# Optimization experiments

Measured on AMD Instinct MI355X. Metric: run time of the kernel, lower is better.

The kernel has to match this reference:

```python
import jax, jax.numpy as jnp
import numpy as np

N_NODES = 50000
N_EDGES = 800000
D_IN = 64
D_OUT = 64


def setup_inputs() -> dict:
    key = jax.random.key(0)
    ks = jax.random.split(key, 5)
    feat = jax.random.normal(ks[0], (N_NODES, D_IN), dtype=jnp.float32)
    src = jax.random.randint(ks[1], (N_EDGES,), 0, N_NODES, dtype=jnp.int64)
    dst = jax.random.randint(ks[2], (N_EDGES,), 0, N_NODES, dtype=jnp.int64)
    # Xavier-uniform-ish scale for weights
    lim = float(np.sqrt(6.0 / (D_IN + D_OUT)) * np.sqrt(2.0))
    W_neigh = jax.random.uniform(ks[3], (D_OUT, D_IN), dtype=jnp.float32, minval=-lim, maxval=lim)
    W_self = jax.random.uniform(ks[4], (D_OUT, D_IN), dtype=jnp.float32, minval=-lim, maxval=lim)
    b_self = jnp.zeros((D_OUT,), dtype=jnp.float32)
    return {"feat": feat, "src": src, "dst": dst,
            "W_neigh": W_neigh, "W_self": W_self, "b_self": b_self}


def reference(feat, src, dst, W_neigh, W_self, b_self):
    # srcdata = fc_neigh(feat_src)  -> [N, D_OUT]
    srcdata = feat @ W_neigh.T
    # A_div.T @ srcdata == mean of transformed source feats over in-edges per dst.
    # deg[j] = A.sum(0)[j]; column scaling by 1/deg then transpose-SpMM.
    agg = jax.ops.segment_sum(srcdata[src], dst, num_segments=N_NODES)  # [N, D_OUT]
    deg = jax.ops.segment_sum(jnp.ones_like(dst, dtype=srcdata.dtype), dst,
                              num_segments=N_NODES)  # [N]
    # Zero-degree columns stay zero in the sparse product (no stored nonzeros).
    dstdata = jnp.where(deg[:, None] > 0, agg / jnp.maximum(deg, 1.0)[:, None], 0.0)
    # rst = fc_self(feat_dst) + dstdata ; feat_dst = feat[:N_dst] = feat (square A)
    return feat @ W_self.T + b_self + dstdata
```

## Files before the change

### kernel.cpp

```cpp
#include <hip/hip_runtime.h>

#define N_NODES 50000
#define N_EDGES 800000
#define D 64
#define RB 128
#define NBUCK 391
#define CAP 3072
#define PAD 16
#define NFEATBLK 3125

typedef __attribute__((ext_vector_type(8))) __bf16 bf16x8;
typedef __attribute__((ext_vector_type(4))) float f32x4;
typedef __attribute__((ext_vector_type(2))) float f32x2;

__device__ inline unsigned f2bf(float f) {
    unsigned b = __builtin_bit_cast(unsigned, f);
    b += 0x7fffu + ((b >> 16) & 1u);
    return b >> 16;
}

__global__ __launch_bounds__(256) void pre_kernel(const float* __restrict__ feat,
                                                  const float* __restrict__ Wn,
                                                  const float* __restrict__ Ws,
                                                  unsigned short* __restrict__ fb,
                                                  unsigned* __restrict__ fq,
                                                  unsigned short* __restrict__ wnb,
                                                  unsigned short* __restrict__ wsb) {
    int b = blockIdx.x;
    int t = threadIdx.x;
    if (b < NFEATBLK) {
        int i = b * 256 + t;
        float4 v = ((const float4*)feat)[i];
        uint2 o;
        o.x = f2bf(v.x) | (f2bf(v.y) << 16);
        o.y = f2bf(v.z) | (f2bf(v.w) << 16);
        ((uint2*)fb)[i] = o;
        int q = __builtin_amdgcn_cvt_pk_fp8_f32(v.x, v.y, 0, false);
        q = __builtin_amdgcn_cvt_pk_fp8_f32(v.z, v.w, q, true);
        fq[i] = (unsigned)q;
    } else {
        for (int i = t; i < D * D; i += 256) {
            wnb[i] = (unsigned short)f2bf(Wn[i]);
            wsb[i] = (unsigned short)f2bf(Ws[i]);
        }
    }
}

__global__ __launch_bounds__(1024) void passB_kernel(const int* __restrict__ src, const int* __restrict__ dst,
                                                     int* __restrict__ bcursor, unsigned int* __restrict__ ebuf) {
    __shared__ int cnt[NBUCK];
    __shared__ int base[NBUCK];
    int t = threadIdx.x;
    for (int i = t; i < NBUCK; i += 1024) cnt[i] = 0;
    __syncthreads();
    int eb = blockIdx.x * 8192;
    int s_[8], b_[8], dl_[8];
#pragma unroll
    for (int k = 0; k < 8; ++k) {
        int e = eb + k * 1024 + t;
        if (e < N_EDGES) {
            int dv = dst[e];
            s_[k] = src[e];
            b_[k] = dv >> 7;
            dl_[k] = dv & (RB - 1);
            atomicAdd(&cnt[b_[k]], 1);
        } else b_[k] = -1;
    }
    __syncthreads();
    for (int i = t; i < NBUCK; i += 1024) {
        int c = cnt[i];
        base[i] = c ? atomicAdd(&bcursor[i * PAD], c) : 0;
    }
    __syncthreads();
#pragma unroll
    for (int k = 0; k < 8; ++k) {
        if (b_[k] >= 0) {
            int pos = atomicAdd(&base[b_[k]], 1);
            if (pos < CAP)
                ebuf[(size_t)b_[k] * CAP + pos] = (unsigned)s_[k] | ((unsigned)dl_[k] << 16);
        }
    }
}

__global__ __launch_bounds__(256) void sort_kernel(const int* __restrict__ bcursor,
                                                   const unsigned int* __restrict__ ebuf,
                                                   unsigned short* __restrict__ es2,
                                                   int* __restrict__ offs, int* __restrict__ degA) {
    __shared__ int cnt[RB];
    __shared__ int sc[RB];
    __shared__ int cur[RB];
    int t = threadIdx.x;
    int bk = blockIdx.x;
    if (t < RB) cnt[t] = 0;
    __syncthreads();
    int s0 = bk * CAP;
    int n = bcursor[bk * PAD];
    if (n > CAP) n = CAP;
    for (int i = t; i < n; i += 256) atomicAdd(&cnt[ebuf[s0 + i] >> 16], 1);
    __syncthreads();
    int c = (t < RB) ? cnt[t] : 0;
    if (t < RB) sc[t] = c;
    __syncthreads();
    for (int d = 1; d < RB; d <<= 1) {
        int v = (t < RB && t >= d) ? sc[t - d] : 0;
        __syncthreads();
        if (t < RB) sc[t] += v;
        __syncthreads();
    }
    if (t < RB) {
        int ex = sc[t] - c;
        cur[t] = ex;
        int node = bk * RB + t;
        if (node < N_NODES) { offs[node] = s0 + ex; degA[node] = c; }
    }
    __syncthreads();
    for (int i = t; i < n; i += 256) {
        unsigned r = ebuf[s0 + i];
        int p = atomicAdd(&cur[r >> 16], 1);
        es2[s0 + p] = (unsigned short)(r & 0xFFFFu);
    }
}

#define ALD 68
__global__ __launch_bounds__(256) void gather_mfma_kernel(
        const unsigned short* __restrict__ fb, const unsigned char* __restrict__ fq,
        const int* __restrict__ offs, const int* __restrict__ degA,
        const unsigned short* __restrict__ es2,
        const unsigned short* __restrict__ wsb, const unsigned short* __restrict__ wnb,
        const float* __restrict__ bias, float* __restrict__ out) {
    __shared__ float agg[16 * ALD];
    int t = threadIdx.x;
    int w = t >> 6, lane = t & 63;
    int es = lane >> 3, p = lane & 7;
    int r0 = blockIdx.x * 16;
#pragma unroll
    for (int q = 0; q < 4; ++q) {
        int nl = w * 4 + q;
        int r = r0 + nl;
        int dg = degA[r];
        int start = offs[r];
        float acc[8] = {0.f, 0.f, 0.f, 0.f, 0.f, 0.f, 0.f, 0.f};
        int i = 0;
        for (; i + 16 <= dg; i += 16) {
            unsigned id0 = es2[start + i + es];
            unsigned id1 = es2[start + i + 8 + es];
            uint2 q0 = *(const uint2*)(fq + (size_t)id0 * D + p * 8);
            uint2 q1 = *(const uint2*)(fq + (size_t)id1 * D + p * 8);
            f32x2 a;
            a = __builtin_amdgcn_cvt_pk_f32_fp8((int)q0.x, false); acc[0] += a.x; acc[1] += a.y;
            a = __builtin_amdgcn_cvt_pk_f32_fp8((int)q0.x, true);  acc[2] += a.x; acc[3] += a.y;
            a = __builtin_amdgcn_cvt_pk_f32_fp8((int)q0.y, false); acc[4] += a.x; acc[5] += a.y;
            a = __builtin_amdgcn_cvt_pk_f32_fp8((int)q0.y, true);  acc[6] += a.x; acc[7] += a.y;
            a = __builtin_amdgcn_cvt_pk_f32_fp8((int)q1.x, false); acc[0] += a.x; acc[1] += a.y;
            a = __builtin_amdgcn_cvt_pk_f32_fp8((int)q1.x, true);  acc[2] += a.x; acc[3] += a.y;
            a = __builtin_amdgcn_cvt_pk_f32_fp8((int)q1.y, false); acc[4] += a.x; acc[5] += a.y;
            a = __builtin_amdgcn_cvt_pk_f32_fp8((int)q1.y, true);  acc[6] += a.x; acc[7] += a.y;
        }
        for (; i + 8 <= dg; i += 8) {
            unsigned id = es2[start + i + es];
            uint2 qv = *(const uint2*)(fq + (size_t)id * D + p * 8);
            f32x2 a;
            a = __builtin_amdgcn_cvt_pk_f32_fp8((int)qv.x, false); acc[0] += a.x; acc[1] += a.y;
            a = __builtin_amdgcn_cvt_pk_f32_fp8((int)qv.x, true);  acc[2] += a.x; acc[3] += a.y;
            a = __builtin_amdgcn_cvt_pk_f32_fp8((int)qv.y, false); acc[4] += a.x; acc[5] += a.y;
            a = __builtin_amdgcn_cvt_pk_f32_fp8((int)qv.y, true);  acc[6] += a.x; acc[7] += a.y;
        }
        int rem = dg - i;
        if (es < rem) {
            unsigned id = es2[start + i + es];
            uint2 qv = *(const uint2*)(fq + (size_t)id * D + p * 8);
            f32x2 a;
            a = __builtin_amdgcn_cvt_pk_f32_fp8((int)qv.x, false); acc[0] += a.x; acc[1] += a.y;
            a = __builtin_amdgcn_cvt_pk_f32_fp8((int)qv.x, true);  acc[2] += a.x; acc[3] += a.y;
            a = __builtin_amdgcn_cvt_pk_f32_fp8((int)qv.y, false); acc[4] += a.x; acc[5] += a.y;
            a = __builtin_amdgcn_cvt_pk_f32_fp8((int)qv.y, true);  acc[6] += a.x; acc[7] += a.y;
        }
#pragma unroll
        for (int m = 8; m <= 32; m <<= 1) {
#pragma unroll
            for (int j = 0; j < 8; ++j) acc[j] += __shfl_xor(acc[j], m);
        }
        if (es == 0) {
            float inv = (dg > 0) ? 1.0f / (float)dg : 0.f;
#pragma unroll
            for (int j = 0; j < 8; ++j) agg[nl * ALD + p * 8 + j] = acc[j] * inv;
        }
    }
    __syncthreads();
    int m = lane & 15, quad = lane >> 4;
    bf16x8 aS0 = *(const bf16x8*)(fb + (size_t)(r0 + m) * D + 0  + quad * 8);
    bf16x8 aS1 = *(const bf16x8*)(fb + (size_t)(r0 + m) * D + 32 + quad * 8);
    bf16x8 aA0, aA1;
#pragma unroll
    for (int j = 0; j < 8; ++j) {
        aA0[j] = (__bf16)agg[m * ALD + 0  + quad * 8 + j];
        aA1[j] = (__bf16)agg[m * ALD + 32 + quad * 8 + j];
    }
    int n = 16 * w + m;
    bf16x8 bS0 = *(const bf16x8*)(wsb + (size_t)n * D + 0  + quad * 8);
    bf16x8 bS1 = *(const bf16x8*)(wsb + (size_t)n * D + 32 + quad * 8);
    bf16x8 bN0 = *(const bf16x8*)(wnb + (size_t)n * D + 0  + quad * 8);
    bf16x8 bN1 = *(const bf16x8*)(wnb + (size_t)n * D + 32 + quad * 8);
    f32x4 acc = {0.f, 0.f, 0.f, 0.f};
    acc = __builtin_amdgcn_mfma_f32_16x16x32_bf16(aS0, bS0, acc, 0, 0, 0);
    acc = __builtin_amdgcn_mfma_f32_16x16x32_bf16(aS1, bS1, acc, 0, 0, 0);
    acc = __builtin_amdgcn_mfma_f32_16x16x32_bf16(aA0, bN0, acc, 0, 0, 0);
    acc = __builtin_amdgcn_mfma_f32_16x16x32_bf16(aA1, bN1, acc, 0, 0, 0);
    float bv = bias[16 * w + m];
#pragma unroll
    for (int reg = 0; reg < 4; ++reg) {
        out[(size_t)(r0 + quad * 4 + reg) * D + 16 * w + m] = acc[reg] + bv;
    }
}

extern "C" void kernel_launch(void* const* d_in, const int* in_sizes, int n_in,
                              void* d_out, int out_size, void* d_ws, size_t ws_size,
                              hipStream_t stream) {
    const float* feat  = (const float*)d_in[0];
    const int*   src   = (const int*)d_in[1];
    const int*   dst   = (const int*)d_in[2];
    const float* Wn    = (const float*)d_in[3];
    const float* Wself = (const float*)d_in[4];
    const float* bself = (const float*)d_in[5];
    float* out = (float*)d_out;

    unsigned short* featb = (unsigned short*)d_ws;
    unsigned*       featq = (unsigned*)(featb + (size_t)N_NODES * D);
    unsigned short* wnb   = (unsigned short*)(featq + (size_t)N_NODES * D / 4);
    unsigned short* wsb   = wnb + D * D;
    unsigned int*   ebuf  = (unsigned int*)(wsb + D * D);
    unsigned short* es2   = (unsigned short*)(ebuf + (size_t)NBUCK * CAP);
    int* bcursor = (int*)(es2 + (size_t)NBUCK * CAP);
    int* offs    = bcursor + NBUCK * PAD;
    int* degA    = offs + N_NODES;

    hipMemsetAsync(bcursor, 0, (size_t)NBUCK * PAD * sizeof(int), stream);

    pre_kernel<<<NFEATBLK + 1, 256, 0, stream>>>(feat, Wn, Wself, featb, featq, wnb, wsb);
    passB_kernel<<<(N_EDGES + 8191) / 8192, 1024, 0, stream>>>(src, dst, bcursor, ebuf);
    sort_kernel<<<NBUCK, 256, 0, stream>>>(bcursor, ebuf, es2, offs, degA);
    gather_mfma_kernel<<<N_NODES / 16, 256, 0, stream>>>(
        featb, (const unsigned char*)featq, offs, degA, es2, wsb, wnb, bself, out);
}
```

Baseline: 129.0 us.

## Remap gather so four threads own one node, removing cross-lane reductions

The gather kernel now assigns four threads per destination node, each loading 16 fp8 features per neighbor as a uint4, so 64 nodes are aggregated per block with no shuffle reductions. Previously a wavefront processed one node at a time and spread edges across lanes with xor-shuffle reductions. Each wave then runs MFMA over all four output column tiles for its 16 rows, and bounds checks handle the partial last block. This cuts shuffle overhead and raises per-thread memory-level parallelism. The cost is load imbalance across threads with different degrees, fewer blocks, and more registers per thread.

```diff
diff --git a/kernel.cpp b/kernel.cpp
--- a/kernel.cpp
+++ b/kernel.cpp
@@ -8,6 +8,8 @@
 #define CAP 3072
 #define PAD 16
 #define NFEATBLK 3125
+#define GN 64
+#define NGBLK 782
 
 typedef __attribute__((ext_vector_type(8))) __bf16 bf16x8;
 typedef __attribute__((ext_vector_type(4))) float f32x4;
@@ -17,6 +19,18 @@
     unsigned b = __builtin_bit_cast(unsigned, f);
     b += 0x7fffu + ((b >> 16) & 1u);
     return b >> 16;
+}
+
+__device__ inline void acc16(float* acc, uint4 v) {
+    f32x2 a;
+    a = __builtin_amdgcn_cvt_pk_f32_fp8((int)v.x, false); acc[0]  += a.x; acc[1]  += a.y;
+    a = __builtin_amdgcn_cvt_pk_f32_fp8((int)v.x, true);  acc[2]  += a.x; acc[3]  += a.y;
+    a = __builtin_amdgcn_cvt_pk_f32_fp8((int)v.y, false); acc[4]  += a.x; acc[5]  += a.y;
+    a = __builtin_amdgcn_cvt_pk_f32_fp8((int)v.y, true);  acc[6]  += a.x; acc[7]  += a.y;
+    a = __builtin_amdgcn_cvt_pk_f32_fp8((int)v.z, false); acc[8]  += a.x; acc[9]  += a.y;
+    a = __builtin_amdgcn_cvt_pk_f32_fp8((int)v.z, true);  acc[10] += a.x; acc[11] += a.y;
+    a = __builtin_amdgcn_cvt_pk_f32_fp8((int)v.w, false); acc[12] += a.x; acc[13] += a.y;
+    a = __builtin_amdgcn_cvt_pk_f32_fp8((int)v.w, true);  acc[14] += a.x; acc[15] += a.y;
 }
 
 __global__ __launch_bounds__(256) void pre_kernel(const float* __restrict__ feat,
@@ -128,88 +142,72 @@
         const unsigned short* __restrict__ es2,
         const unsigned short* __restrict__ wsb, const unsigned short* __restrict__ wnb,
         const float* __restrict__ bias, float* __restrict__ out) {
-    __shared__ float agg[16 * ALD];
-    int t = threadIdx.x;
+    __shared__ float agg[GN * ALD];
+    int t = threadIdx.x;
+    int ns = t >> 2, p = t & 3;
+    int r0 = blockIdx.x * GN;
+    int r = r0 + ns;
+    int dg = 0, start = 0;
+    if (r < N_NODES) { dg = degA[r]; start = offs[r]; }
+    float acc[16];
+#pragma unroll
+    for (int j = 0; j < 16; ++j) acc[j] = 0.f;
+    const unsigned char* fqp = fq + p * 16;
+    int i = 0;
+    for (; i + 4 <= dg; i += 4) {
+        unsigned id0 = es2[start + i + 0];
+        unsigned id1 = es2[start + i + 1];
+        unsigned id2 = es2[start + i + 2];
+        unsigned id3 = es2[start + i + 3];
+        uint4 v0 = *(const uint4*)(fqp + (size_t)id0 * D);
+        uint4 v1 = *(const uint4*)(fqp + (size_t)id1 * D);
+        uint4 v2 = *(const uint4*)(fqp + (size_t)id2 * D);
+        uint4 v3 = *(const uint4*)(fqp + (size_t)id3 * D);
+        acc16(acc, v0); acc16(acc, v1); acc16(acc, v2); acc16(acc, v3);
+    }
+    for (; i < dg; ++i) {
+        unsigned id = es2[start + i];
+        uint4 v = *(const uint4*)(fqp + (size_t)id * D);
+        acc16(acc, v);
+    }
+    float inv = (dg > 0) ? 1.0f / (float)dg : 0.f;
+#pragma unroll
+    for (int j = 0; j < 16; j += 4) {
+        float4 o = make_float4(acc[j] * inv, acc[j + 1] * inv, acc[j + 2] * inv, acc[j + 3] * inv);
+        *(float4*)(&agg[ns * ALD + p * 16 + j]) = o;
+    }
+    __syncthreads();
     int w = t >> 6, lane = t & 63;
-    int es = lane >> 3, p = lane & 7;
-    int r0 = blockIdx.x * 16;
-#pragma unroll
-    for (int q = 0; q < 4; ++q) {
-        int nl = w * 4 + q;
-        int r = r0 + nl;
-        int dg = degA[r];
-        int start = offs[r];
-        float acc[8] = {0.f, 0.f, 0.f, 0.f, 0.f, 0.f, 0.f, 0.f};
-        int i = 0;
-        for (; i + 16 <= dg; i += 16) {
-            unsigned id0 = es2[start + i + es];
-            unsigned id1 = es2[start + i + 8 + es];
-            uint2 q0 = *(const uint2*)(fq + (size_t)id0 * D + p * 8);
-            uint2 q1 = *(const uint2*)(fq + (size_t)id1 * D + p * 8);
-            f32x2 a;
-            a = __builtin_amdgcn_cvt_pk_f32_fp8((int)q0.x, false); acc[0] += a.x; acc[1] += a.y;
-            a = __builtin_amdgcn_cvt_pk_f32_fp8((int)q0.x, true);  acc[2] += a.x; acc[3] += a.y;
-            a = __builtin_amdgcn_cvt_pk_f32_fp8((int)q0.y, false); acc[4] += a.x; acc[5] += a.y;
-            a = __builtin_amdgcn_cvt_pk_f32_fp8((int)q0.y, true);  acc[6] += a.x; acc[7] += a.y;
-            a = __builtin_amdgcn_cvt_pk_f32_fp8((int)q1.x, false); acc[0] += a.x; acc[1] += a.y;
-            a = __builtin_amdgcn_cvt_pk_f32_fp8((int)q1.x, true);  acc[2] += a.x; acc[3] += a.y;
-            a = __builtin_amdgcn_cvt_pk_f32_fp8((int)q1.y, false); acc[4] += a.x; acc[5] += a.y;
-            a = __builtin_amdgcn_cvt_pk_f32_fp8((int)q1.y, true);  acc[6] += a.x; acc[7] += a.y;
+    int m = lane & 15, quad = lane >> 4;
+    int row = r0 + 16 * w + m;
+    int rowA = row < N_NODES ? row : N_NODES - 1;
+    bf16x8 aS0 = *(const bf16x8*)(fb + (size_t)rowA * D + 0  + quad * 8);
+    bf16x8 aS1 = *(const bf16x8*)(fb + (size_t)rowA * D + 32 + quad * 8);
+    bf16x8 aA0, aA1;
+#pragma unroll
+    for (int j = 0; j < 8; ++j) {
+        aA0[j] = (__bf16)agg[(16 * w + m) * ALD + 0  + quad * 8 + j];
+        aA1[j] = (__bf16)agg[(16 * w + m) * ALD + 32 + quad * 8 + j];
+    }
+#pragma unroll
+    for (int tt = 0; tt < 4; ++tt) {
+        int n = 16 * tt + m;
+        bf16x8 bS0 = *(const bf16x8*)(wsb + (size_t)n * D + 0  + quad * 8);
+        bf16x8 bS1 = *(const bf16x8*)(wsb + (size_t)n * D + 32 + quad * 8);
+        bf16x8 bN0 = *(const bf16x8*)(wnb + (size_t)n * D + 0  + quad * 8);
+        bf16x8 bN1 = *(const bf16x8*)(wnb + (size_t)n * D + 32 + quad * 8);
+        f32x4 c = {0.f, 0.f, 0.f, 0.f};
+        c = __builtin_amdgcn_mfma_f32_16x16x32_bf16(aS0, bS0, c, 0, 0, 0);
+        c = __builtin_amdgcn_mfma_f32_16x16x32_bf16(aS1, bS1, c, 0, 0, 0);
+        c = __builtin_amdgcn_mfma_f32_16x16x32_bf16(aA0, bN0, c, 0, 0, 0);
+        c = __builtin_amdgcn_mfma_f32_16x16x32_bf16(aA1, bN1, c, 0, 0, 0);
+        float bv = bias[16 * tt + m];
+#pragma unroll
+        for (int reg = 0; reg < 4; ++reg) {
+            int orow = r0 + 16 * w + quad * 4 + reg;
+            if (orow < N_NODES)
+                out[(size_t)orow * D + 16 * tt + m] = c[reg] + bv;
         }
-        for (; i + 8 <= dg; i += 8) {
-            unsigned id = es2[start + i + es];
-            uint2 qv = *(const uint2*)(fq + (size_t)id * D + p * 8);
-            f32x2 a;
-            a = __builtin_amdgcn_cvt_pk_f32_fp8((int)qv.x, false); acc[0] += a.x; acc[1] += a.y;
-            a = __builtin_amdgcn_cvt_pk_f32_fp8((int)qv.x, true);  acc[2] += a.x; acc[3] += a.y;
-            a = __builtin_amdgcn_cvt_pk_f32_fp8((int)qv.y, false); acc[4] += a.x; acc[5] += a.y;
-            a = __builtin_amdgcn_cvt_pk_f32_fp8((int)qv.y, true);  acc[6] += a.x; acc[7] += a.y;
-        }
-        int rem = dg - i;
-        if (es < rem) {
-            unsigned id = es2[start + i + es];
-            uint2 qv = *(const uint2*)(fq + (size_t)id * D + p * 8);
-            f32x2 a;
-            a = __builtin_amdgcn_cvt_pk_f32_fp8((int)qv.x, false); acc[0] += a.x; acc[1] += a.y;
-            a = __builtin_amdgcn_cvt_pk_f32_fp8((int)qv.x, true);  acc[2] += a.x; acc[3] += a.y;
-            a = __builtin_amdgcn_cvt_pk_f32_fp8((int)qv.y, false); acc[4] += a.x; acc[5] += a.y;
-            a = __builtin_amdgcn_cvt_pk_f32_fp8((int)qv.y, true);  acc[6] += a.x; acc[7] += a.y;
-        }
-#pragma unroll
-        for (int m = 8; m <= 32; m <<= 1) {
-#pragma unroll
-            for (int j = 0; j < 8; ++j) acc[j] += __shfl_xor(acc[j], m);
-        }
-        if (es == 0) {
-            float inv = (dg > 0) ? 1.0f / (float)dg : 0.f;
-#pragma unroll
-            for (int j = 0; j < 8; ++j) agg[nl * ALD + p * 8 + j] = acc[j] * inv;
-        }
-    }
-    __syncthreads();
-    int m = lane & 15, quad = lane >> 4;
-    bf16x8 aS0 = *(const bf16x8*)(fb + (size_t)(r0 + m) * D + 0  + quad * 8);
-    bf16x8 aS1 = *(const bf16x8*)(fb + (size_t)(r0 + m) * D + 32 + quad * 8);
-    bf16x8 aA0, aA1;
-#pragma unroll
-    for (int j = 0; j < 8; ++j) {
-        aA0[j] = (__bf16)agg[m * ALD + 0  + quad * 8 + j];
-        aA1[j] = (__bf16)agg[m * ALD + 32 + quad * 8 + j];
-    }
-    int n = 16 * w + m;
-    bf16x8 bS0 = *(const bf16x8*)(wsb + (size_t)n * D + 0  + quad * 8);
-    bf16x8 bS1 = *(const bf16x8*)(wsb + (size_t)n * D + 32 + quad * 8);
-    bf16x8 bN0 = *(const bf16x8*)(wnb + (size_t)n * D + 0  + quad * 8);
-    bf16x8 bN1 = *(const bf16x8*)(wnb + (size_t)n * D + 32 + quad * 8);
-    f32x4 acc = {0.f, 0.f, 0.f, 0.f};
-    acc = __builtin_amdgcn_mfma_f32_16x16x32_bf16(aS0, bS0, acc, 0, 0, 0);
-    acc = __builtin_amdgcn_mfma_f32_16x16x32_bf16(aS1, bS1, acc, 0, 0, 0);
-    acc = __builtin_amdgcn_mfma_f32_16x16x32_bf16(aA0, bN0, acc, 0, 0, 0);
-    acc = __builtin_amdgcn_mfma_f32_16x16x32_bf16(aA1, bN1, acc, 0, 0, 0);
-    float bv = bias[16 * w + m];
-#pragma unroll
-    for (int reg = 0; reg < 4; ++reg) {
-        out[(size_t)(r0 + quad * 4 + reg) * D + 16 * w + m] = acc[reg] + bv;
     }
 }
 
@@ -239,6 +237,6 @@
     pre_kernel<<<NFEATBLK + 1, 256, 0, stream>>>(feat, Wn, Wself, featb, featq, wnb, wsb);
     passB_kernel<<<(N_EDGES + 8191) / 8192, 1024, 0, stream>>>(src, dst, bcursor, ebuf);
     sort_kernel<<<NBUCK, 256, 0, stream>>>(bcursor, ebuf, es2, offs, degA);
-    gather_mfma_kernel<<<N_NODES / 16, 256, 0, stream>>>(
+    gather_mfma_kernel<<<NGBLK, 256, 0, stream>>>(
         featb, (const unsigned char*)featq, offs, degA, es2, wsb, wnb, bself, out);
 }
```

Result: faster. 121.9 us (-5.4%).
